# Performance work log

Hardware: AMD Instinct MI355X
Metric: run time of the kernel (lower is better)

## Reference

```python
import jax, jax.numpy as jnp
import numpy as np

N_NODES = 50000
N_EDGES = 800000
IN_DIM = 100
HIDDEN = 16
N_CLASSES = 40


def setup_inputs() -> dict:
    key = jax.random.key(0)
    k1, k2, k3, k4, k5, k6 = jax.random.split(key, 6)
    features = jax.random.normal(k1, (N_NODES, IN_DIM), dtype=jnp.float32)
    edge_src = jax.random.randint(k2, (N_EDGES,), 0, N_NODES, dtype=jnp.int32)
    edge_dst = jax.random.randint(k3, (N_EDGES,), 0, N_NODES, dtype=jnp.int32)
    edge_vals = jax.random.uniform(k4, (N_EDGES,), dtype=jnp.float32)
    W1 = jax.random.uniform(k5, (IN_DIM, HIDDEN), dtype=jnp.float32)
    W2 = jax.random.uniform(k6, (HIDDEN, N_CLASSES), dtype=jnp.float32)
    return {"features": features, "edge_src": edge_src, "edge_dst": edge_dst,
            "edge_vals": edge_vals, "W1": W1, "W2": W2}


def _spmm(edge_src, edge_dst, edge_vals, x):
    # z = A @ x with A given as (dst, src, val) edge list; equivalent to the
    # partition-loop addmm accumulation in broadcast().
    msgs = edge_vals[:, None] * x[edge_src]            # [E, d]
    return jax.ops.segment_sum(msgs, edge_dst, num_segments=x.shape[0])


def reference(features, edge_src, edge_dst, edge_vals, W1, W2):
    h = jax.nn.relu(_spmm(edge_src, edge_dst, edge_vals, features) @ W1)  # [N, 16]
    out = _spmm(edge_src, edge_dst, edge_vals, h) @ W2                    # [N, C]
    return jax.nn.log_softmax(out, axis=1)
```

## Files before the change

### kernel.cpp

```cpp
#include <hip/hip_runtime.h>

#define N_NODES   50000
#define N_EDGES   800000
#define IN_DIM    100
#define HIDDEN    16
#define N_CLASSES 40

#define BSHIFT 6
#define NPB    64
#define NBKT   782
#define PB     256
#define EPB    3125
#define EPT    7
#define CAP    2048
#define GEMMB  782

#define K1_LDS 33456

__global__ __launch_bounds__(512) void build_and_gemm(const int* __restrict__ src,
                                                      const int* __restrict__ dst,
                                                      const float* __restrict__ val,
                                                      const float* __restrict__ X,
                                                      const float* __restrict__ W,
                                                      int* __restrict__ BTt,
                                                      int2* __restrict__ binned,
                                                      float* __restrict__ Y) {
    __shared__ __align__(16) char smem[K1_LDS];
    const int tid = threadIdx.x;

    if (blockIdx.x < PB) {
        int*  cnt    = (int*)smem;
        int*  lcur   = (int*)(smem + 3200);
        int*  wpre   = (int*)(smem + 6400);
        int2* staged = (int2*)(smem + 8448);
        const int b = blockIdx.x, e0 = b * EPB;
        const int lane = tid & 63, w = tid >> 6;

        for (int k = tid; k < NBKT; k += 512) cnt[k] = 0;
        __syncthreads();

        int pk[EPT], ps[EPT]; float pv[EPT];
#pragma unroll
        for (int q = 0; q < EPT; ++q) {
            const int i = tid + q * 512;
            if (i < EPB) {
                const int e = e0 + i;
                const int d = dst[e];
                pk[q] = d >> BSHIFT;
                ps[q] = src[e] | ((d & (NPB - 1)) << 16);
                pv[q] = val[e];
                atomicAdd(&cnt[pk[q]], 1);
            } else pk[q] = -1;
        }
        __syncthreads();

        const int k0 = 2 * tid, k1 = 2 * tid + 1;
        const int a  = (k0 < NBKT) ? cnt[k0] : 0;
        const int bb = (k1 < NBKT) ? cnt[k1] : 0;
        const int s  = a + bb;
        int x = s;
#pragma unroll
        for (int d = 1; d < 64; d <<= 1) {
            const int y = __shfl_up(x, d, 64);
            if (lane >= d) x += y;
        }
        if (lane == 63) wpre[w] = x;
        __syncthreads();
        int add = 0;
        for (int i = 0; i < w; ++i) add += wpre[i];
        const int excl = add + x - s;
        if (k0 < NBKT) { lcur[k0] = excl;     BTt[k0 * PB + b] = excl; }
        if (k1 < NBKT) { lcur[k1] = excl + a; BTt[k1 * PB + b] = excl + a; }
        if (tid == 0)  BTt[NBKT * PB + b] = EPB;
        __syncthreads();

#pragma unroll
        for (int q = 0; q < EPT; ++q) {
            if (pk[q] >= 0) {
                const int pos = atomicAdd(&lcur[pk[q]], 1);
                staged[pos] = make_int2(ps[q], __float_as_int(pv[q]));
            }
        }
        __syncthreads();

        for (int i = tid; i < EPB; i += 512)
            binned[e0 + i] = staged[i];
    } else {
        float* sX = (float*)smem;
        float* sW = (float*)(smem + 25600);
        const int b2   = blockIdx.x - PB;
        const int row0 = b2 * 64;
        const int nrows = min(64, N_NODES - row0);

        const float4* W4 = (const float4*)W;
        float4* sW4 = (float4*)sW;
        for (int i = tid; i < (IN_DIM * HIDDEN) / 4; i += 512) sW4[i] = W4[i];
        const float4* X4 = (const float4*)(X + (size_t)row0 * IN_DIM);
        float4* sX4 = (float4*)sX;
        const int nf4 = nrows * (IN_DIM / 4);
        for (int i = tid; i < nf4; i += 512) sX4[i] = X4[i];
        __syncthreads();

        const int r = tid >> 3, hh = tid & 7;
        if (r >= nrows) return;
        float2 acc = make_float2(0.f, 0.f);
        const float* xr = &sX[r * IN_DIM];
#pragma unroll
        for (int kk = 0; kk < IN_DIM; ++kk) {
            const float xk = xr[kk];
            const float2 wv = *(const float2*)&sW[kk * HIDDEN + hh * 2];
            acc.x = fmaf(xk, wv.x, acc.x);
            acc.y = fmaf(xk, wv.y, acc.y);
        }
        *(float2*)&Y[(size_t)(row0 + r) * HIDDEN + hh * 2] = acc;
    }
}

__device__ __forceinline__ int bucket_sort_lds(const int* __restrict__ BTt,
                                               const int2* __restrict__ binned,
                                               int k, int tid,
                                               int2* raw, int2* srt,
                                               int* cnt, int* cur, int* aux) {
    const int lane = tid & 63, w = tid >> 6;
    if (tid < NPB) cnt[tid] = 0;

    const int rs = BTt[k * PB + tid];
    const int re = BTt[(k + 1) * PB + tid];
    const int len = re - rs;
    int x = len;
#pragma unroll
    for (int d = 1; d < 64; d <<= 1) {
        const int y = __shfl_up(x, d, 64);
        if (lane >= d) x += y;
    }
    if (lane == 63) aux[w] = x;
    __syncthreads();
    int add = 0;
    for (int i = 0; i < w; ++i) add += aux[i];
    const int tot = aux[0] + aux[1] + aux[2] + aux[3];

    int o = add + x - len;
    const int2* rb = binned + (size_t)tid * EPB;
    for (int p = rs; p < re; ++p, ++o) raw[o] = rb[p];
    __syncthreads();

    for (int i = tid; i < tot; i += 256)
        atomicAdd(&cnt[(raw[i].x >> 16) & (NPB - 1)], 1);
    __syncthreads();

    if (tid < NPB) {
        const int v = cnt[tid];
        int xx = v;
#pragma unroll
        for (int d = 1; d < 64; d <<= 1) {
            const int y = __shfl_up(xx, d, 64);
            if (tid >= d) xx += y;
        }
        cur[tid] = xx - v;
    }
    __syncthreads();

    for (int i = tid; i < tot; i += 256) {
        const int2 e = raw[i];
        const int pos = atomicAdd(&cur[(e.x >> 16) & (NPB - 1)], 1);
        srt[pos] = make_int2(e.x & 0xFFFF, e.y);
    }
    __syncthreads();
    return tot;
}

__device__ __forceinline__ float4 gather4(const int2* srt, int beg, int deg,
                                          const float4* X4, int q) {
    float4 a = make_float4(0.f, 0.f, 0.f, 0.f);
    int p = beg;
    for (; p + 2 <= beg + deg; p += 2) {
        const int2 e0 = srt[p];
        const int2 e1 = srt[p + 1];
        const float v0 = __int_as_float(e0.y);
        const float v1 = __int_as_float(e1.y);
        const float4 x0 = X4[(size_t)e0.x * 4 + q];
        const float4 x1 = X4[(size_t)e1.x * 4 + q];
        a.x = fmaf(v0, x0.x, a.x); a.y = fmaf(v0, x0.y, a.y);
        a.z = fmaf(v0, x0.z, a.z); a.w = fmaf(v0, x0.w, a.w);
        a.x = fmaf(v1, x1.x, a.x); a.y = fmaf(v1, x1.y, a.y);
        a.z = fmaf(v1, x1.z, a.z); a.w = fmaf(v1, x1.w, a.w);
    }
    if (p < beg + deg) {
        const int2 e = srt[p];
        const float v = __int_as_float(e.y);
        const float4 xv = X4[(size_t)e.x * 4 + q];
        a.x = fmaf(v, xv.x, a.x); a.y = fmaf(v, xv.y, a.y);
        a.z = fmaf(v, xv.z, a.z); a.w = fmaf(v, xv.w, a.w);
    }
    return a;
}

__global__ __launch_bounds__(256) void sort_gather1(const int* __restrict__ BTt,
                                                    const int2* __restrict__ binned,
                                                    const float* __restrict__ Yin,
                                                    float* __restrict__ Z) {
    __shared__ int2 raw[CAP];
    __shared__ int2 srt[CAP];
    __shared__ int  cnt[NPB], cur[NPB], aux[4];
    const int tid = threadIdx.x, k = blockIdx.x;

    bucket_sort_lds(BTt, binned, k, tid, raw, srt, cnt, cur, aux);

    const int g = tid >> 2, q = tid & 3;
    const int node = k * NPB + g;
    const int deg = cnt[g];
    const int beg = cur[g] - deg;
    float4 a = gather4(srt, beg, deg, (const float4*)Yin, q);
    if (node < N_NODES) {
        a.x = fmaxf(a.x, 0.f); a.y = fmaxf(a.y, 0.f);
        a.z = fmaxf(a.z, 0.f); a.w = fmaxf(a.w, 0.f);
        ((float4*)Z)[(size_t)node * 4 + q] = a;
    }
}

__global__ __launch_bounds__(256) void sort_gather_out(const int* __restrict__ BTt,
                                                       const int2* __restrict__ binned,
                                                       const float* __restrict__ Zin,
                                                       const float* __restrict__ W2,
                                                       float* __restrict__ out) {
    __shared__ int2  raw[CAP];
    __shared__ int2  srt[CAP];
    __shared__ int   cnt[NPB], cur[NPB], aux[4];
    __shared__ float sW2[HIDDEN * N_CLASSES];
    __shared__ float zt[NPB * 17];
    const int tid = threadIdx.x, k = blockIdx.x;

    for (int i = tid; i < HIDDEN * N_CLASSES; i += 256) sW2[i] = W2[i];

    bucket_sort_lds(BTt, binned, k, tid, raw, srt, cnt, cur, aux);

    const int g = tid >> 2, q = tid & 3;
    const int node = k * NPB + g;
    const int deg = cnt[g];
    const int beg = cur[g] - deg;
    const float4 a = gather4(srt, beg, deg, (const float4*)Zin, q);
    zt[g * 17 + q * 4 + 0] = a.x;
    zt[g * 17 + q * 4 + 1] = a.y;
    zt[g * 17 + q * 4 + 2] = a.z;
    zt[g * 17 + q * 4 + 3] = a.w;
    __syncthreads();

    if (node >= N_NODES) return;

    float z[HIDDEN];
#pragma unroll
    for (int kk = 0; kk < HIDDEN; ++kk) z[kk] = zt[g * 17 + kk];

    float oc[10];
#pragma unroll
    for (int c = 0; c < 10; ++c) oc[c] = 0.f;
#pragma unroll
    for (int kk = 0; kk < HIDDEN; ++kk) {
        const float zk = z[kk];
        const float* wr = &sW2[kk * N_CLASSES + q * 10];
#pragma unroll
        for (int c = 0; c < 10; ++c) oc[c] = fmaf(zk, wr[c], oc[c]);
    }
    float m = oc[0];
#pragma unroll
    for (int c = 1; c < 10; ++c) m = fmaxf(m, oc[c]);
#pragma unroll
    for (int d = 1; d < 4; d <<= 1) m = fmaxf(m, __shfl_xor(m, d, 4));
    float se = 0.f;
#pragma unroll
    for (int c = 0; c < 10; ++c) se += __expf(oc[c] - m);
#pragma unroll
    for (int d = 1; d < 4; d <<= 1) se += __shfl_xor(se, d, 4);
    const float lse = m + __logf(se);

    float* orow = out + (size_t)node * N_CLASSES + q * 10;
#pragma unroll
    for (int c = 0; c < 10; ++c) orow[c] = oc[c] - lse;
}

extern "C" void kernel_launch(void* const* d_in, const int* in_sizes, int n_in,
                              void* d_out, int out_size, void* d_ws, size_t ws_size,
                              hipStream_t stream) {
    const float* features = (const float*)d_in[0];
    const int*   edge_src = (const int*)d_in[1];
    const int*   edge_dst = (const int*)d_in[2];
    const float* edge_val = (const float*)d_in[3];
    const float* W1       = (const float*)d_in[4];
    const float* W2       = (const float*)d_in[5];
    float*       out      = (float*)d_out;

    char* base = (char*)d_ws;
    const size_t HNB = (size_t)N_NODES * HIDDEN * sizeof(float);
    float* y1     = (float*)(base);
    float* z1     = (float*)(base + HNB);
    int2*  binned = (int2*) (base + 2 * HNB);
    int*   BTt    = (int*)  (base + 2 * HNB + (size_t)N_EDGES * 8);

    build_and_gemm<<<PB + GEMMB, 512, 0, stream>>>(edge_src, edge_dst, edge_val,
                                                   features, W1, BTt, binned, y1);
    sort_gather1<<<NBKT, 256, 0, stream>>>(BTt, binned, y1, z1);
    sort_gather_out<<<NBKT, 256, 0, stream>>>(BTt, binned, z1, W2, out);
}
```

Baseline: 128.6 us.

## Fuse histogram into raw copy, unroll gather by four, shuffle instead of LDS transpose

Bucket counts are now taken while edges are copied into LDS, which removes one pass over the staged edges and one barrier. The gather loop is unrolled to four edges so more independent global loads are in flight. The output kernel exchanges the per-node hidden vector through lane shuffles instead of an LDS staging array and barrier. CAP is reduced to shrink LDS use and allow more blocks per CU, at the risk of overflow if a bucket ever holds more than 1792 edges.

```diff
diff --git a/kernel.cpp b/kernel.cpp
--- a/kernel.cpp
+++ b/kernel.cpp
@@ -12,7 +12,7 @@
 #define PB     256
 #define EPB    3125
 #define EPT    7
-#define CAP    2048
+#define CAP    1792
 #define GEMMB  782
 
 #define K1_LDS 33456
@@ -116,11 +116,11 @@
     }
 }
 
-__device__ __forceinline__ int bucket_sort_lds(const int* __restrict__ BTt,
-                                               const int2* __restrict__ binned,
-                                               int k, int tid,
-                                               int2* raw, int2* srt,
-                                               int* cnt, int* cur, int* aux) {
+__device__ __forceinline__ void bucket_sort_lds(const int* __restrict__ BTt,
+                                                const int2* __restrict__ binned,
+                                                int k, int tid,
+                                                int2* raw, int2* srt,
+                                                int* cnt, int* cur, int* aux) {
     const int lane = tid & 63, w = tid >> 6;
     if (tid < NPB) cnt[tid] = 0;
 
@@ -137,15 +137,14 @@
     __syncthreads();
     int add = 0;
     for (int i = 0; i < w; ++i) add += aux[i];
-    const int tot = aux[0] + aux[1] + aux[2] + aux[3];
 
     int o = add + x - len;
     const int2* rb = binned + (size_t)tid * EPB;
-    for (int p = rs; p < re; ++p, ++o) raw[o] = rb[p];
-    __syncthreads();
-
-    for (int i = tid; i < tot; i += 256)
-        atomicAdd(&cnt[(raw[i].x >> 16) & (NPB - 1)], 1);
+    for (int p = rs; p < re; ++p, ++o) {
+        const int2 e = rb[p];
+        raw[o] = e;
+        atomicAdd(&cnt[(e.x >> 16) & (NPB - 1)], 1);
+    }
     __syncthreads();
 
     if (tid < NPB) {
@@ -160,32 +159,41 @@
     }
     __syncthreads();
 
+    const int tot = aux[0] + aux[1] + aux[2] + aux[3];
     for (int i = tid; i < tot; i += 256) {
         const int2 e = raw[i];
         const int pos = atomicAdd(&cur[(e.x >> 16) & (NPB - 1)], 1);
         srt[pos] = make_int2(e.x & 0xFFFF, e.y);
     }
     __syncthreads();
-    return tot;
 }
 
 __device__ __forceinline__ float4 gather4(const int2* srt, int beg, int deg,
                                           const float4* X4, int q) {
     float4 a = make_float4(0.f, 0.f, 0.f, 0.f);
+    const int end = beg + deg;
     int p = beg;
-    for (; p + 2 <= beg + deg; p += 2) {
+    for (; p + 4 <= end; p += 4) {
         const int2 e0 = srt[p];
         const int2 e1 = srt[p + 1];
-        const float v0 = __int_as_float(e0.y);
-        const float v1 = __int_as_float(e1.y);
+        const int2 e2 = srt[p + 2];
+        const int2 e3 = srt[p + 3];
         const float4 x0 = X4[(size_t)e0.x * 4 + q];
         const float4 x1 = X4[(size_t)e1.x * 4 + q];
+        const float4 x2 = X4[(size_t)e2.x * 4 + q];
+        const float4 x3 = X4[(size_t)e3.x * 4 + q];
+        const float v0 = __int_as_float(e0.y), v1 = __int_as_float(e1.y);
+        const float v2 = __int_as_float(e2.y), v3 = __int_as_float(e3.y);
         a.x = fmaf(v0, x0.x, a.x); a.y = fmaf(v0, x0.y, a.y);
         a.z = fmaf(v0, x0.z, a.z); a.w = fmaf(v0, x0.w, a.w);
         a.x = fmaf(v1, x1.x, a.x); a.y = fmaf(v1, x1.y, a.y);
         a.z = fmaf(v1, x1.z, a.z); a.w = fmaf(v1, x1.w, a.w);
-    }
-    if (p < beg + deg) {
+        a.x = fmaf(v2, x2.x, a.x); a.y = fmaf(v2, x2.y, a.y);
+        a.z = fmaf(v2, x2.z, a.z); a.w = fmaf(v2, x2.w, a.w);
+        a.x = fmaf(v3, x3.x, a.x); a.y = fmaf(v3, x3.y, a.y);
+        a.z = fmaf(v3, x3.z, a.z); a.w = fmaf(v3, x3.w, a.w);
+    }
+    for (; p < end; ++p) {
         const int2 e = srt[p];
         const float v = __int_as_float(e.y);
         const float4 xv = X4[(size_t)e.x * 4 + q];
@@ -227,7 +235,6 @@
     __shared__ int2  srt[CAP];
     __shared__ int   cnt[NPB], cur[NPB], aux[4];
     __shared__ float sW2[HIDDEN * N_CLASSES];
-    __shared__ float zt[NPB * 17];
     const int tid = threadIdx.x, k = blockIdx.x;
 
     for (int i = tid; i < HIDDEN * N_CLASSES; i += 256) sW2[i] = W2[i];
@@ -239,17 +246,20 @@
     const int deg = cnt[g];
     const int beg = cur[g] - deg;
     const float4 a = gather4(srt, beg, deg, (const float4*)Zin, q);
-    zt[g * 17 + q * 4 + 0] = a.x;
-    zt[g * 17 + q * 4 + 1] = a.y;
-    zt[g * 17 + q * 4 + 2] = a.z;
-    zt[g * 17 + q * 4 + 3] = a.w;
-    __syncthreads();
 
     if (node >= N_NODES) return;
 
     float z[HIDDEN];
 #pragma unroll
-    for (int kk = 0; kk < HIDDEN; ++kk) z[kk] = zt[g * 17 + kk];
+    for (int qq = 0; qq < 4; ++qq) {
+        float4 b;
+        b.x = __shfl(a.x, qq, 4);
+        b.y = __shfl(a.y, qq, 4);
+        b.z = __shfl(a.z, qq, 4);
+        b.w = __shfl(a.w, qq, 4);
+        z[4 * qq + 0] = b.x; z[4 * qq + 1] = b.y;
+        z[4 * qq + 2] = b.z; z[4 * qq + 3] = b.w;
+    }
 
     float oc[10];
 #pragma unroll
```

Result: no change. 129.2 us (+0.5%).
